# Kernel optimization log

Measured on AMD Instinct MI355X. Metric: run time of the kernel, lower is better.

Reference implementation:

```python
import jax, jax.numpy as jnp
import numpy as np

N, C, H, O, NUM_CLASSES = 4096, 768, 512, 50, 1


def setup_inputs() -> dict:
    key = jax.random.key(0)
    ks = jax.random.split(key, 8)
    x = jax.random.normal(ks[0], (N, C), dtype=jnp.float32)
    labels = jax.random.randint(ks[1], (N,), 0, 2, dtype=jnp.int64)
    W1 = jax.random.normal(ks[2], (C, H), dtype=jnp.float32) / np.sqrt(C)
    b1 = jnp.zeros((H,), dtype=jnp.float32)
    W2 = jax.random.normal(ks[3], (H, O), dtype=jnp.float32) / np.sqrt(H)
    b2 = jnp.zeros((O,), dtype=jnp.float32)
    fcW = jax.random.normal(ks[4], (C + O, NUM_CLASSES), dtype=jnp.float32) / np.sqrt(C + O)
    fcb = jnp.zeros((NUM_CLASSES,), dtype=jnp.float32)
    return {"x": x, "labels": labels, "W1": W1, "b1": b1, "W2": W2, "b2": b2, "fcW": fcW, "fcb": fcb}


def _build_graph(x, labels):
    # similarity-threshold edge construction (dense masked form of the python double loop)
    sim = x @ x.T                                   # [N, N]
    n = x.shape[0]
    diff = labels[:, None] != labels[None, :]       # cross-label pairs
    cnt = jnp.sum(diff)
    s = jnp.sum(jnp.where(diff, sim, 0.0))
    threshold = jnp.where(cnt > 0, s / cnt.astype(sim.dtype), jnp.asarray(0.0, sim.dtype))
    eye = jnp.eye(n, dtype=bool)
    same = (labels[:, None] == labels[None, :]) & ~eye
    edge_mask = same & (sim <= threshold)           # symmetric (sim symmetric)
    loss_mask = edge_mask & (jnp.arange(n)[:, None] < jnp.arange(n)[None, :])  # i<j pairs
    adj = jax.lax.stop_gradient(edge_mask.astype(x.dtype))
    # GCN normalization with self-loops
    a = adj + jnp.eye(n, dtype=x.dtype)
    dinv = jax.lax.rsqrt(jnp.sum(a, axis=1))        # deg >= 1
    norm_adj = dinv[:, None] * a * dinv[None, :]
    return norm_adj, loss_mask


def reference(x, labels, W1, b1, W2, b2, fcW, fcb):
    norm_adj, loss_mask = _build_graph(x, labels)
    h = jax.nn.relu(norm_adj @ (x @ W1) + b1)       # conv1 + relu
    g = norm_adj @ (h @ W2) + b2                    # conv2
    f_g = jnp.concatenate([x, g], axis=-1)          # [N, C+O]
    out = f_g @ fcW + fcb                           # [N, 1]
    return out, f_g, loss_mask, x
```

## Files before the change

### kernel.cpp

```cpp
#include <hip/hip_runtime.h>
#include <hip/hip_bf16.h>
#include <math.h>

#define NN 4096
#define CD 768
#define HD 512
#define OD 50
#define FGD 818

typedef short short8 __attribute__((ext_vector_type(8)));
typedef float f32x4 __attribute__((ext_vector_type(4)));
typedef unsigned short us4 __attribute__((ext_vector_type(4)));
typedef unsigned short ushortT;
typedef unsigned char uchar;

__device__ inline ushortT f2bf(float v) {
    __hip_bfloat16 b = __float2bfloat16(v);
    return *(ushortT*)&b;
}
__device__ inline float bf2f(ushortT u) {
    __hip_bfloat16 b = *(__hip_bfloat16*)&u;
    return __bfloat162float(b);
}
__device__ inline float dinv_of(int d) {
    return (float)(1.0 / sqrt((double)(1 + d)));
}

__global__ __launch_bounds__(256) void gsum_kernel(const float* __restrict__ x,
                                                   const int* __restrict__ labels,
                                                   double* __restrict__ gsum) {
    int b = blockIdx.x;
    int t = threadIdx.x;
    double a0[3] = {0, 0, 0}, a1[3] = {0, 0, 0};
    for (int rr = 0; rr < 16; ++rr) {
        int row = b * 16 + rr;
        int lab = labels[row];
#pragma unroll
        for (int s = 0; s < 3; ++s) {
            double v = (double)x[(size_t)row * CD + t + s * 256];
            if (lab == 0) a0[s] += v; else a1[s] += v;
        }
    }
#pragma unroll
    for (int s = 0; s < 3; ++s) {
        atomicAdd(&gsum[t + s * 256], a0[s]);
        atomicAdd(&gsum[768 + t + s * 256], a1[s]);
    }
}

__global__ __launch_bounds__(256) void gdot_kernel(const double* __restrict__ gsum,
                                                   const int* __restrict__ labels,
                                                   double* __restrict__ scal) {
    int t = threadIdx.x;
    double d = 0.0;
    for (int c = t; c < CD; c += 256) d += gsum[c] * gsum[768 + c];
    int n0 = 0;
    for (int i = t; i < NN; i += 256) n0 += (labels[i] == 0) ? 1 : 0;
    for (int off = 32; off; off >>= 1) {
        d += __shfl_down(d, off);
        n0 += __shfl_down(n0, off);
    }
    __shared__ double sd[4];
    __shared__ int sn[4];
    int wid = t >> 6, lane = t & 63;
    if (lane == 0) { sd[wid] = d; sn[wid] = n0; }
    __syncthreads();
    if (t == 0) {
        double D = sd[0] + sd[1] + sd[2] + sd[3];
        double N0 = (double)(sn[0] + sn[1] + sn[2] + sn[3]);
        scal[0] = 2.0 * D;
        scal[1] = 2.0 * N0 * ((double)NN - N0);
    }
}

#define BAND 4e-3
#define RC_CAP (1 << 18)

__global__ __launch_bounds__(256) void sim_fused(
    const ushortT* __restrict__ xh, const ushortT* __restrict__ xl,
    const int* __restrict__ labels, const double* __restrict__ scal,
    ushortT* __restrict__ ab, float* __restrict__ lm, int* __restrict__ deg,
    int* __restrict__ rc_cnt, int* __restrict__ rc_list) {
    int t = blockIdx.x;
    int by = (int)((129.0 - sqrt(16641.0 - 8.0 * (double)t)) * 0.5);
    while (by * (129 - by) / 2 > t) --by;
    while ((by + 1) * (129 - (by + 1)) / 2 <= t) ++by;
    int bx = by + (t - by * (129 - by) / 2);
    bool diag = (bx == by);

    __shared__ ushortT lds[4 * 64 * 72];
    __shared__ int larr[128];
    int tid = threadIdx.x;
    int lane = tid & 63;
    int w = tid >> 6;
    int wr = w >> 1, wc = w & 1;
    int m = lane & 15, quad = lane >> 4;
    int row0 = by * 64, col0 = bx * 64;

    if (tid < 64) larr[tid] = labels[row0 + tid];
    else if (tid < 128) larr[tid] = labels[col0 + tid - 64];

    f32x4 acc[2][2] = {{{0.f, 0.f, 0.f, 0.f}, {0.f, 0.f, 0.f, 0.f}},
                       {{0.f, 0.f, 0.f, 0.f}, {0.f, 0.f, 0.f, 0.f}}};

    for (int k0 = 0; k0 < CD; k0 += 64) {
#pragma unroll
        for (int tt = 0; tt < 2; ++tt) {
            int id2 = tid + tt * 256;
            int row = id2 >> 3, c8 = (id2 & 7) * 8;
            *(short8*)&lds[0 * 4608 + row * 72 + c8] =
                *(const short8*)&xh[(size_t)(row0 + row) * CD + k0 + c8];
            *(short8*)&lds[1 * 4608 + row * 72 + c8] =
                *(const short8*)&xl[(size_t)(row0 + row) * CD + k0 + c8];
            *(short8*)&lds[2 * 4608 + row * 72 + c8] =
                *(const short8*)&xh[(size_t)(col0 + row) * CD + k0 + c8];
            *(short8*)&lds[3 * 4608 + row * 72 + c8] =
                *(const short8*)&xl[(size_t)(col0 + row) * CD + k0 + c8];
        }
        __syncthreads();
#pragma unroll
        for (int ks = 0; ks < 2; ++ks) {
            short8 ah[2], al[2], bh[2], bl[2];
#pragma unroll
            for (int i = 0; i < 2; ++i) {
                int ro = (wr * 32 + i * 16 + m) * 72 + ks * 32 + quad * 8;
                ah[i] = *(const short8*)&lds[0 * 4608 + ro];
                al[i] = *(const short8*)&lds[1 * 4608 + ro];
            }
#pragma unroll
            for (int j = 0; j < 2; ++j) {
                int co = (wc * 32 + j * 16 + m) * 72 + ks * 32 + quad * 8;
                bh[j] = *(const short8*)&lds[2 * 4608 + co];
                bl[j] = *(const short8*)&lds[3 * 4608 + co];
            }
#pragma unroll
            for (int i = 0; i < 2; ++i)
#pragma unroll
                for (int j = 0; j < 2; ++j) {
                    acc[i][j] = __builtin_amdgcn_mfma_f32_16x16x32_bf16(
                        ah[i], bh[j], acc[i][j], 0, 0, 0);
                    acc[i][j] = __builtin_amdgcn_mfma_f32_16x16x32_bf16(
                        ah[i], bl[j], acc[i][j], 0, 0, 0);
                    acc[i][j] = __builtin_amdgcn_mfma_f32_16x16x32_bf16(
                        al[i], bh[j], acc[i][j], 0, 0, 0);
                }
        }
        __syncthreads();
    }

    double thrd;
    {
        double cnt = scal[1];
        thrd = (cnt > 0.0) ? (scal[0] / cnt) : 0.0;
    }
    uchar* flags = (uchar*)lds;
#pragma unroll
    for (int i = 0; i < 2; ++i)
#pragma unroll
        for (int j = 0; j < 2; ++j) {
#pragma unroll
            for (int r = 0; r < 4; ++r) {
                int row = wr * 32 + i * 16 + quad * 4 + r;
                int col = wc * 32 + j * 16 + m;
                bool same = (larr[row] == larr[64 + col]);
                bool selfp = ((row0 + row) == (col0 + col));
                bool edge = false;
                if (same && !selfp) {
                    double s = (double)acc[i][j][r];
                    if (s <= thrd - BAND) {
                        edge = true;
                    } else if (s <= thrd + BAND) {
                        edge = (s <= thrd);
                        int enc = ((row0 + row) << 12) | (col0 + col) |
                                  (diag ? 0 : (1 << 24)) |
                                  (edge ? (1 << 25) : 0);
                        int idx = atomicAdd(rc_cnt, 1);
                        if (idx < RC_CAP) rc_list[idx] = enc;
                    }
                }
                flags[row * 68 + col] = edge ? 1 : 0;
            }
        }
    __syncthreads();

    {
        int r = tid >> 2, q = tid & 3;
        int cnti = 0;
#pragma unroll
        for (int s = 0; s < 4; ++s) {
            int cb = q * 16 + s * 4;
            float4 f;
            us4 a4;
#pragma unroll
            for (int k2 = 0; k2 < 4; ++k2) {
                int c = cb + k2;
                bool fl = flags[r * 68 + c] != 0;
                cnti += fl ? 1 : 0;
                ((ushortT*)&a4)[k2] =
                    (fl || (diag && r == c)) ? (ushortT)0x3F80 : (ushortT)0;
                ((float*)&f)[k2] = (fl && (row0 + r < col0 + c)) ? 1.0f : 0.0f;
            }
            *(us4*)&ab[(size_t)(row0 + r) * NN + col0 + cb] = a4;
            *(float4*)&lm[(size_t)(row0 + r) * NN + col0 + cb] = f;
        }
        cnti += __shfl_down(cnti, 1);
        cnti += __shfl_down(cnti, 2);
        if (q == 0 && cnti) atomicAdd(&deg[row0 + r], cnti);
    }

    if (!diag) {
        int c = tid >> 2, q = tid & 3;
        int cnti = 0;
        float4 fz = {0.0f, 0.0f, 0.0f, 0.0f};
#pragma unroll
        for (int s = 0; s < 4; ++s) {
            int rb = q * 16 + s * 4;
            us4 a4;
#pragma unroll
            for (int k2 = 0; k2 < 4; ++k2) {
                bool fl = flags[(rb + k2) * 68 + c] != 0;
                cnti += fl ? 1 : 0;
                ((ushortT*)&a4)[k2] = fl ? (ushortT)0x3F80 : (ushortT)0;
            }
            *(us4*)&ab[(size_t)(col0 + c) * NN + row0 + rb] = a4;
            *(float4*)&lm[(size_t)(col0 + c) * NN + row0 + rb] = fz;
        }
        cnti += __shfl_down(cnti, 1);
        cnti += __shfl_down(cnti, 2);
        if (q == 0 && cnti) atomicAdd(&deg[col0 + c], cnti);
    }
}

__global__ __launch_bounds__(256) void rc_fix(
    const float* __restrict__ x, const double* __restrict__ scal,
    const int* __restrict__ rc_cnt, const int* __restrict__ rc_list,
    ushortT* __restrict__ ab, float* __restrict__ lm, int* __restrict__ deg) {
    int cnt = *rc_cnt;
    if (cnt > RC_CAP) cnt = RC_CAP;
    double thrd;
    {
        double c = scal[1];
        thrd = (c > 0.0) ? (scal[0] / c) : 0.0;
    }
    int lane = threadIdx.x & 63;
    int wid = (blockIdx.x * 256 + threadIdx.x) >> 6;
    int nw = (gridDim.x * 256) >> 6;
    for (int e = wid; e < cnt; e += nw) {
        int enc = rc_list[e];
        int c = enc & 0xFFF;
        int r = (enc >> 12) & 0xFFF;
        bool mirror = (enc >> 24) & 1;
        bool prov = (enc >> 25) & 1;
        const float* xi = x + (size_t)r * CD;
        const float* xj = x + (size_t)c * CD;
        double d = 0.0;
#pragma unroll
        for (int s = 0; s < 12; ++s)
            d += (double)xi[lane + s * 64] * (double)xj[lane + s * 64];
        for (int off = 32; off; off >>= 1) d += __shfl_down(d, off);
        if (lane == 0) {
            bool exact = (d <= thrd);
            if (exact != prov) {
                ushortT av = exact ? (ushortT)0x3F80 : (ushortT)0;
                ab[(size_t)r * NN + c] = av;
                lm[(size_t)r * NN + c] = (exact && r < c) ? 1.0f : 0.0f;
                int dlt = exact ? 1 : -1;
                atomicAdd(&deg[r], dlt);
                if (mirror) {
                    ab[(size_t)c * NN + r] = av;
                    atomicAdd(&deg[c], dlt);
                }
            }
        }
    }
}

__global__ __launch_bounds__(256) void prep_kernel(
    const float* __restrict__ x, const float* __restrict__ W1,
    const float* __restrict__ W2, float* __restrict__ fg, float* __restrict__ xo,
    ushortT* __restrict__ xh, ushortT* __restrict__ xl, ushortT* __restrict__ w1t,
    ushortT* __restrict__ w2t) {
    int b = blockIdx.x;
    if (b < 4096) {
        int t = threadIdx.x;
        if (t < 192) {
            float4 v = *(const float4*)&x[(size_t)b * CD + t * 4];
            *(float4*)&xo[(size_t)b * CD + t * 4] = v;
            fg[(size_t)b * FGD + t * 4 + 0] = v.x;
            fg[(size_t)b * FGD + t * 4 + 1] = v.y;
            fg[(size_t)b * FGD + t * 4 + 2] = v.z;
            fg[(size_t)b * FGD + t * 4 + 3] = v.w;
            us4 hh, ll;
            float* vp = (float*)&v;
#pragma unroll
            for (int k = 0; k < 4; ++k) {
                ushortT h = f2bf(vp[k]);
                ((ushortT*)&hh)[k] = h;
                ((ushortT*)&ll)[k] = f2bf(vp[k] - bf2f(h));
            }
            *(us4*)&xh[(size_t)b * CD + t * 4] = hh;
            *(us4*)&xl[(size_t)b * CD + t * 4] = ll;
        }
        return;
    }
    __shared__ float tT[32][33];
    const float* P;
    ushortT* T;
    int K, N, Npad, k0, n0;
    if (b < 4480) {
        int bb = b - 4096;
        P = W1; T = w1t; K = CD; N = HD; Npad = HD;
        k0 = (bb % 24) * 32; n0 = (bb / 24) * 32;
    } else {
        int bb = b - 4480;
        P = W2; T = w2t; K = HD; N = OD; Npad = 64;
        k0 = (bb % 16) * 32; n0 = (bb / 16) * 32;
    }
    int tx = threadIdx.x & 31, ty = threadIdx.x >> 5;
#pragma unroll
    for (int s = 0; s < 4; ++s) {
        int k = k0 + ty + s * 8, n = n0 + tx;
        tT[ty + s * 8][tx] = (k < K && n < N) ? P[(size_t)k * N + n] : 0.0f;
    }
    __syncthreads();
#pragma unroll
    for (int s = 0; s < 4; ++s) {
        int n = n0 + ty + s * 8, k = k0 + tx;
        if (n < Npad && k < K) T[(size_t)n * K + k] = f2bf(tT[tx][ty + s * 8]);
    }
}

template <bool RELU, bool HASBIAS, int EPI>
__global__ __launch_bounds__(256) void gemm_bf16(
    const ushortT* __restrict__ A, const ushortT* __restrict__ B,
    ushortT* __restrict__ Cb, int M, int Nn, int K, int ldc,
    const int* __restrict__ deg, const float* __restrict__ bias) {
    __shared__ ushortT lds[2 * 64 * 72];
    int tid = threadIdx.x;
    int lane = tid & 63;
    int w = tid >> 6;
    int wr = w >> 1, wc = w & 1;
    int m = lane & 15, quad = lane >> 4;
    int row0 = blockIdx.y * 64, col0 = blockIdx.x * 64;

    f32x4 acc[2][2] = {{{0.f, 0.f, 0.f, 0.f}, {0.f, 0.f, 0.f, 0.f}},
                       {{0.f, 0.f, 0.f, 0.f}, {0.f, 0.f, 0.f, 0.f}}};

    for (int k0 = 0; k0 < K; k0 += 64) {
#pragma unroll
        for (int t = 0; t < 2; ++t) {
            int id2 = tid + t * 256;
            int row = id2 >> 3, c8 = (id2 & 7) * 8;
            *(short8*)&lds[row * 72 + c8] =
                *(const short8*)&A[(size_t)(row0 + row) * K + k0 + c8];
            *(short8*)&lds[4608 + row * 72 + c8] =
                *(const short8*)&B[(size_t)(col0 + row) * K + k0 + c8];
        }
        __syncthreads();
#pragma unroll
        for (int ks = 0; ks < 2; ++ks) {
            short8 af[2], bf[2];
#pragma unroll
            for (int i = 0; i < 2; ++i)
                af[i] = *(const short8*)&lds[(wr * 32 + i * 16 + m) * 72 +
                                             ks * 32 + quad * 8];
#pragma unroll
            for (int j = 0; j < 2; ++j)
                bf[j] = *(const short8*)&lds[4608 + (wc * 32 + j * 16 + m) * 72 +
                                             ks * 32 + quad * 8];
#pragma unroll
            for (int i = 0; i < 2; ++i)
#pragma unroll
                for (int j = 0; j < 2; ++j)
                    acc[i][j] = __builtin_amdgcn_mfma_f32_16x16x32_bf16(
                        af[i], bf[j], acc[i][j], 0, 0, 0);
        }
        __syncthreads();
    }

    if (EPI == 2) {
        ushortT* Th = lds;
#pragma unroll
        for (int i = 0; i < 2; ++i)
#pragma unroll
            for (int j = 0; j < 2; ++j)
#pragma unroll
                for (int r = 0; r < 4; ++r) {
                    int row = wr * 32 + i * 16 + quad * 4 + r;
                    int col = wc * 32 + j * 16 + m;
                    float dv = dinv_of(deg[row0 + row]);
                    Th[col * 72 + row] = f2bf(acc[i][j][r] * dv);
                }
        __syncthreads();
#pragma unroll
        for (int t = 0; t < 2; ++t) {
            int id2 = tid + t * 256;
            int cc = id2 >> 3, chunk = id2 & 7;
            *(short8*)&Cb[(size_t)(col0 + cc) * M + row0 + chunk * 8] =
                *(const short8*)&Th[cc * 72 + chunk * 8];
        }
    } else {
#pragma unroll
        for (int i = 0; i < 2; ++i)
#pragma unroll
            for (int j = 0; j < 2; ++j)
#pragma unroll
                for (int r = 0; r < 4; ++r) {
                    int row = wr * 32 + i * 16 + quad * 4 + r;
                    int col = wc * 32 + j * 16 + m;
                    int gr = row0 + row, gc = col0 + col;
                    if (gc < Nn) {
                        float v = acc[i][j][r] * dinv_of(deg[gr]);
                        if (HASBIAS) v += bias[gc];
                        if (RELU) v = fmaxf(v, 0.0f);
                        Cb[(size_t)gr * ldc + gc] = f2bf(v);
                    }
                }
    }
}

__global__ __launch_bounds__(256) void gemm_part(
    const ushortT* __restrict__ A, const ushortT* __restrict__ B,
    float* __restrict__ P, int M, int K, int KC) {
    __shared__ ushortT lds[2 * 64 * 72];
    int tid = threadIdx.x;
    int lane = tid & 63;
    int w = tid >> 6;
    int wr = w >> 1, wc = w & 1;
    int m = lane & 15, quad = lane >> 4;
    int kb = blockIdx.x;
    int row0 = blockIdx.y * 64;
    int kbase = kb * KC;

    f32x4 acc[2][2] = {{{0.f, 0.f, 0.f, 0.f}, {0.f, 0.f, 0.f, 0.f}},
                       {{0.f, 0.f, 0.f, 0.f}, {0.f, 0.f, 0.f, 0.f}}};

    for (int k0 = 0; k0 < KC; k0 += 64) {
#pragma unroll
        for (int t = 0; t < 2; ++t) {
            int id2 = tid + t * 256;
            int row = id2 >> 3, c8 = (id2 & 7) * 8;
            *(short8*)&lds[row * 72 + c8] =
                *(const short8*)&A[(size_t)(row0 + row) * K + kbase + k0 + c8];
            *(short8*)&lds[4608 + row * 72 + c8] =
                *(const short8*)&B[(size_t)row * K + kbase + k0 + c8];
        }
        __syncthreads();
#pragma unroll
        for (int ks = 0; ks < 2; ++ks) {
            short8 af[2], bf[2];
#pragma unroll
            for (int i = 0; i < 2; ++i)
                af[i] = *(const short8*)&lds[(wr * 32 + i * 16 + m) * 72 +
                                             ks * 32 + quad * 8];
#pragma unroll
            for (int j = 0; j < 2; ++j)
                bf[j] = *(const short8*)&lds[4608 + (wc * 32 + j * 16 + m) * 72 +
                                             ks * 32 + quad * 8];
#pragma unroll
            for (int i = 0; i < 2; ++i)
#pragma unroll
                for (int j = 0; j < 2; ++j)
                    acc[i][j] = __builtin_amdgcn_mfma_f32_16x16x32_bf16(
                        af[i], bf[j], acc[i][j], 0, 0, 0);
        }
        __syncthreads();
    }
#pragma unroll
    for (int i = 0; i < 2; ++i)
#pragma unroll
        for (int j = 0; j < 2; ++j)
#pragma unroll
            for (int r = 0; r < 4; ++r) {
                int row = wr * 32 + i * 16 + quad * 4 + r;
                int col = wc * 32 + j * 16 + m;
                P[((size_t)kb * M + row0 + row) * 64 + col] = acc[i][j][r];
            }
}

__global__ __launch_bounds__(256) void gemm_partW(
    const ushortT* __restrict__ A, const ushortT* __restrict__ B,
    float* __restrict__ P, int M, int K, int KC, int ldP) {
    __shared__ ushortT lds[2 * 64 * 72];
    int tid = threadIdx.x;
    int lane = tid & 63;
    int w = tid >> 6;
    int wr = w >> 1, wc = w & 1;
    int m = lane & 15, quad = lane >> 4;
    int col0 = blockIdx.x * 64;
    int row0 = blockIdx.y * 64;
    int kb = blockIdx.z;
    int kbase = kb * KC;

    f32x4 acc[2][2] = {{{0.f, 0.f, 0.f, 0.f}, {0.f, 0.f, 0.f, 0.f}},
                       {{0.f, 0.f, 0.f, 0.f}, {0.f, 0.f, 0.f, 0.f}}};

    for (int k0 = 0; k0 < KC; k0 += 64) {
#pragma unroll
        for (int t = 0; t < 2; ++t) {
            int id2 = tid + t * 256;
            int row = id2 >> 3, c8 = (id2 & 7) * 8;
            *(short8*)&lds[row * 72 + c8] =
                *(const short8*)&A[(size_t)(row0 + row) * K + kbase + k0 + c8];
            *(short8*)&lds[4608 + row * 72 + c8] =
                *(const short8*)&B[(size_t)(col0 + row) * K + kbase + k0 + c8];
        }
        __syncthreads();
#pragma unroll
        for (int ks = 0; ks < 2; ++ks) {
            short8 af[2], bf[2];
#pragma unroll
            for (int i = 0; i < 2; ++i)
                af[i] = *(const short8*)&lds[(wr * 32 + i * 16 + m) * 72 +
                                             ks * 32 + quad * 8];
#pragma unroll
            for (int j = 0; j < 2; ++j)
                bf[j] = *(const short8*)&lds[4608 + (wc * 32 + j * 16 + m) * 72 +
                                             ks * 32 + quad * 8];
#pragma unroll
            for (int i = 0; i < 2; ++i)
#pragma unroll
                for (int j = 0; j < 2; ++j)
                    acc[i][j] = __builtin_amdgcn_mfma_f32_16x16x32_bf16(
                        af[i], bf[j], acc[i][j], 0, 0, 0);
        }
        __syncthreads();
    }
#pragma unroll
    for (int i = 0; i < 2; ++i)
#pragma unroll
        for (int j = 0; j < 2; ++j)
#pragma unroll
            for (int r = 0; r < 4; ++r) {
                int row = wr * 32 + i * 16 + quad * 4 + r;
                int col = wc * 32 + j * 16 + m;
                P[((size_t)kb * M + row0 + row) * ldP + col0 + col] =
                    acc[i][j][r];
            }
}

__global__ __launch_bounds__(256) void k5_epi(const float* __restrict__ P5,
                                              const int* __restrict__ deg,
                                              const float* __restrict__ b1,
                                              ushortT* __restrict__ hb) {
    int tid = threadIdx.x;
    int cg = tid & 127;
    int rr = tid >> 7;
#pragma unroll
    for (int p = 0; p < 2; ++p) {
        int r = blockIdx.x * 4 + p * 2 + rr;
        float dv = dinv_of(deg[r]);
        float4 s = {0.f, 0.f, 0.f, 0.f};
#pragma unroll
        for (int kb = 0; kb < 4; ++kb) {
            float4 v = *(const float4*)&P5[((size_t)kb * NN + r) * HD + cg * 4];
            s.x += v.x; s.y += v.y; s.z += v.z; s.w += v.w;
        }
        float4 bv = *(const float4*)&b1[cg * 4];
        us4 o;
        o[0] = f2bf(fmaxf(s.x * dv + bv.x, 0.f));
        o[1] = f2bf(fmaxf(s.y * dv + bv.y, 0.f));
        o[2] = f2bf(fmaxf(s.z * dv + bv.z, 0.f));
        o[3] = f2bf(fmaxf(s.w * dv + bv.w, 0.f));
        *(us4*)&hb[(size_t)r * HD + cg * 4] = o;
    }
}

__global__ __launch_bounds__(256) void k6_epi(const float* __restrict__ P6,
                                              const int* __restrict__ deg,
                                              ushortT* __restrict__ hw2sT) {
    __shared__ ushortT Th[64 * 72];
    int row0 = blockIdx.x * 64;
    int tid = threadIdx.x;
    int rl = tid >> 2, q = tid & 3;
    float dv = dinv_of(deg[row0 + rl]);
#pragma unroll
    for (int s = 0; s < 16; ++s) {
        int c = q * 16 + s;
        float v = 0.f;
#pragma unroll
        for (int kb = 0; kb < 4; ++kb)
            v += P6[((size_t)kb * NN + row0 + rl) * 64 + c];
        Th[c * 72 + rl] = f2bf(v * dv);
    }
    __syncthreads();
#pragma unroll
    for (int t = 0; t < 2; ++t) {
        int id2 = tid + t * 256;
        int cc = id2 >> 3, chunk = id2 & 7;
        *(short8*)&hw2sT[(size_t)cc * NN + row0 + chunk * 8] =
            *(const short8*)&Th[cc * 72 + chunk * 8];
    }
}

__global__ __launch_bounds__(256) void k7_epi_out(
    const float* __restrict__ P7, const int* __restrict__ deg,
    const float* __restrict__ b2, const float* __restrict__ fcW,
    const float* __restrict__ fcb, float* __restrict__ fg,
    float* __restrict__ out) {
    int row0 = blockIdx.x * 64;
    int tid = threadIdx.x;
    int rl = tid >> 2, q = tid & 3;
    int r = row0 + rl;
    float dv = dinv_of(deg[r]);
    float sg = 0.f;
#pragma unroll
    for (int s = 0; s < 16; ++s) {
        int c = q * 16 + s;
        if (c < OD) {
            float v = 0.f;
#pragma unroll
            for (int kb = 0; kb < 8; ++kb)
                v += P7[((size_t)kb * NN + r) * 64 + c];
            v = v * dv + b2[c];
            fg[(size_t)r * FGD + CD + c] = v;
            sg += v * fcW[CD + c];
        }
    }
    const float* fr = fg + (size_t)r * FGD;
    float sx = 0.f;
    for (int k = q * 192; k < (q + 1) * 192; k += 2) {
        float2 vv = *(const float2*)&fr[k];
        float2 ww = *(const float2*)&fcW[k];
        sx += vv.x * ww.x + vv.y * ww.y;
    }
    float s = sx + sg;
    s += __shfl_down(s, 1);
    s += __shfl_down(s, 2);
    if (q == 0) out[r] = s + fcb[0];
}

extern "C" void kernel_launch(void* const* d_in, const int* in_sizes, int n_in,
                              void* d_out, int out_size, void* d_ws, size_t ws_size,
                              hipStream_t stream) {
    const float* x = (const float*)d_in[0];
    const int* labels = (const int*)d_in[1];
    const float* W1 = (const float*)d_in[2];
    const float* b1 = (const float*)d_in[3];
    const float* W2 = (const float*)d_in[4];
    const float* b2 = (const float*)d_in[5];
    const float* fcW = (const float*)d_in[6];
    const float* fcb = (const float*)d_in[7];
    float* outp = (float*)d_out;

    const size_t o_out = 0;
    const size_t o_fg = 4096;
    const size_t o_lm = o_fg + (size_t)NN * FGD;
    const size_t o_x = o_lm + (size_t)NN * NN;

    char* ws = (char*)d_ws;
    size_t off = 0;
    ushortT* ab = (ushortT*)(ws + off); off += (size_t)NN * NN * 2;
    ushortT* xh = (ushortT*)(ws + off); off += (size_t)NN * CD * 2;
    ushortT* xl = (ushortT*)(ws + off); off += (size_t)NN * CD * 2;
    ushortT* w1t = (ushortT*)(ws + off); off += (size_t)HD * CD * 2;
    ushortT* xw1sT = (ushortT*)(ws + off); off += (size_t)HD * NN * 2;
    ushortT* hb = (ushortT*)(ws + off); off += (size_t)NN * HD * 2;
    ushortT* w2t = (ushortT*)(ws + off); off += (size_t)64 * HD * 2;
    ushortT* hw2sT = (ushortT*)(ws + off); off += (size_t)64 * NN * 2;
    char* zbase = ws + off;
    int* deg = (int*)(ws + off); off += (size_t)NN * 4;
    double* gsum = (double*)(ws + off); off += 1536 * 8;
    double* scal = (double*)(ws + off); off += 16;
    int* rc_cnt = (int*)(ws + off); off += 16;
    size_t zbytes = (size_t)NN * 4 + 1536 * 8 + 16 + 16;
    char* uni = ws + off;
    int* rc_list = (int*)uni;
    float* P5 = (float*)uni;
    float* P6 = (float*)uni;
    float* P7 = (float*)uni;
    off += (size_t)4 * NN * HD * 4;

    hipMemsetAsync(zbase, 0, zbytes, stream);

    prep_kernel<<<4512, 256, 0, stream>>>(x, W1, W2, outp + o_fg, outp + o_x, xh, xl,
                                          w1t, w2t);

    gsum_kernel<<<256, 256, 0, stream>>>(x, labels, gsum);
    gdot_kernel<<<1, 256, 0, stream>>>(gsum, labels, scal);

    sim_fused<<<2080, 256, 0, stream>>>(xh, xl, labels, scal, ab, outp + o_lm, deg,
                                        rc_cnt, rc_list);

    rc_fix<<<512, 256, 0, stream>>>(x, scal, rc_cnt, rc_list, ab, outp + o_lm, deg);

    gemm_bf16<false, false, 2><<<dim3(HD / 64, NN / 64), 256, 0, stream>>>(
        xh, w1t, xw1sT, NN, HD, CD, 0, deg, nullptr);

    gemm_partW<<<dim3(HD / 64, NN / 64, 4), 256, 0, stream>>>(
        ab, xw1sT, P5, NN, NN, NN / 4, HD);
    k5_epi<<<NN / 4, 256, 0, stream>>>(P5, deg, b1, hb);

    gemm_part<<<dim3(4, NN / 64), 256, 0, stream>>>(hb, w2t, P6, NN, HD, HD / 4);
    k6_epi<<<NN / 64, 256, 0, stream>>>(P6, deg, hw2sT);

    gemm_part<<<dim3(8, NN / 64), 256, 0, stream>>>(ab, hw2sT, P7, NN, NN, NN / 8);
    k7_epi_out<<<NN / 64, 256, 0, stream>>>(P7, deg, b2, fcW, fcb, outp + o_fg,
                                            outp + o_out);
}
```

Measured before the change: 354.8 us.

## Store adjacency as packed bitmask and expand to bf16 inside GEMM loaders

The dense bf16 adjacency matrix (32 MB) is replaced by a 1-bit-per-entry packed u64 bitmask (2 MB). The similarity kernel now writes these bits, and the fixup kernel updates them with atomicOr and atomicAnd. Both adjacency GEMMs expand the bits to bf16 1.0/0.0 in LDS while staging tiles. This cuts the traffic of writing the adjacency once and reading it twice, at the cost of extra ALU work for unpacking and 64-bit atomics in the fixup path.

```diff
diff --git a/kernel.cpp b/kernel.cpp
--- a/kernel.cpp
+++ b/kernel.cpp
@@ -13,6 +13,7 @@
 typedef unsigned short us4 __attribute__((ext_vector_type(4)));
 typedef unsigned short ushortT;
 typedef unsigned char uchar;
+typedef unsigned long long u64;
 
 __device__ inline ushortT f2bf(float v) {
     __hip_bfloat16 b = __float2bfloat16(v);
@@ -79,7 +80,7 @@
 __global__ __launch_bounds__(256) void sim_fused(
     const ushortT* __restrict__ xh, const ushortT* __restrict__ xl,
     const int* __restrict__ labels, const double* __restrict__ scal,
-    ushortT* __restrict__ ab, float* __restrict__ lm, int* __restrict__ deg,
+    u64* __restrict__ abbits, float* __restrict__ lm, int* __restrict__ deg,
     int* __restrict__ rc_cnt, int* __restrict__ rc_list) {
     int t = blockIdx.x;
     int by = (int)((129.0 - sqrt(16641.0 - 8.0 * (double)t)) * 0.5);
@@ -186,55 +187,68 @@
     {
         int r = tid >> 2, q = tid & 3;
         int cnti = 0;
+        unsigned int bits16 = 0;
 #pragma unroll
         for (int s = 0; s < 4; ++s) {
             int cb = q * 16 + s * 4;
             float4 f;
-            us4 a4;
 #pragma unroll
             for (int k2 = 0; k2 < 4; ++k2) {
                 int c = cb + k2;
                 bool fl = flags[r * 68 + c] != 0;
                 cnti += fl ? 1 : 0;
-                ((ushortT*)&a4)[k2] =
-                    (fl || (diag && r == c)) ? (ushortT)0x3F80 : (ushortT)0;
+                if (fl || (diag && r == c)) bits16 |= 1u << (s * 4 + k2);
                 ((float*)&f)[k2] = (fl && (row0 + r < col0 + c)) ? 1.0f : 0.0f;
             }
-            *(us4*)&ab[(size_t)(row0 + r) * NN + col0 + cb] = a4;
             *(float4*)&lm[(size_t)(row0 + r) * NN + col0 + cb] = f;
         }
+        unsigned int s1 = __shfl_down(bits16, 1);
+        unsigned int s2 = __shfl_down(bits16, 2);
+        unsigned int s3 = __shfl_down(bits16, 3);
         cnti += __shfl_down(cnti, 1);
         cnti += __shfl_down(cnti, 2);
-        if (q == 0 && cnti) atomicAdd(&deg[row0 + r], cnti);
+        if (q == 0) {
+            u64 u = (u64)bits16 | ((u64)s1 << 16) | ((u64)s2 << 32) |
+                    ((u64)s3 << 48);
+            abbits[(size_t)(row0 + r) * 64 + bx] = u;
+            if (cnti) atomicAdd(&deg[row0 + r], cnti);
+        }
     }
 
     if (!diag) {
         int c = tid >> 2, q = tid & 3;
         int cnti = 0;
+        unsigned int bits16 = 0;
         float4 fz = {0.0f, 0.0f, 0.0f, 0.0f};
 #pragma unroll
         for (int s = 0; s < 4; ++s) {
             int rb = q * 16 + s * 4;
-            us4 a4;
 #pragma unroll
             for (int k2 = 0; k2 < 4; ++k2) {
                 bool fl = flags[(rb + k2) * 68 + c] != 0;
                 cnti += fl ? 1 : 0;
-                ((ushortT*)&a4)[k2] = fl ? (ushortT)0x3F80 : (ushortT)0;
-            }
-            *(us4*)&ab[(size_t)(col0 + c) * NN + row0 + rb] = a4;
+                if (fl) bits16 |= 1u << (s * 4 + k2);
+            }
             *(float4*)&lm[(size_t)(col0 + c) * NN + row0 + rb] = fz;
         }
+        unsigned int s1 = __shfl_down(bits16, 1);
+        unsigned int s2 = __shfl_down(bits16, 2);
+        unsigned int s3 = __shfl_down(bits16, 3);
         cnti += __shfl_down(cnti, 1);
         cnti += __shfl_down(cnti, 2);
-        if (q == 0 && cnti) atomicAdd(&deg[col0 + c], cnti);
+        if (q == 0) {
+            u64 u = (u64)bits16 | ((u64)s1 << 16) | ((u64)s2 << 32) |
+                    ((u64)s3 << 48);
+            abbits[(size_t)(col0 + c) * 64 + by] = u;
+            if (cnti) atomicAdd(&deg[col0 + c], cnti);
+        }
     }
 }
 
 __global__ __launch_bounds__(256) void rc_fix(
     const float* __restrict__ x, const double* __restrict__ scal,
     const int* __restrict__ rc_cnt, const int* __restrict__ rc_list,
-    ushortT* __restrict__ ab, float* __restrict__ lm, int* __restrict__ deg) {
+    u64* __restrict__ abbits, float* __restrict__ lm, int* __restrict__ deg) {
     int cnt = *rc_cnt;
     if (cnt > RC_CAP) cnt = RC_CAP;
     double thrd;
@@ -261,13 +275,16 @@
         if (lane == 0) {
             bool exact = (d <= thrd);
             if (exact != prov) {
-                ushortT av = exact ? (ushortT)0x3F80 : (ushortT)0;
-                ab[(size_t)r * NN + c] = av;
+                u64 mk = 1ull << (c & 63);
+                if (exact) atomicOr(&abbits[(size_t)r * 64 + (c >> 6)], mk);
+                else       atomicAnd(&abbits[(size_t)r * 64 + (c >> 6)], ~mk);
                 lm[(size_t)r * NN + c] = (exact && r < c) ? 1.0f : 0.0f;
                 int dlt = exact ? 1 : -1;
                 atomicAdd(&deg[r], dlt);
                 if (mirror) {
-                    ab[(size_t)c * NN + r] = av;
+                    u64 mk2 = 1ull << (r & 63);
+                    if (exact) atomicOr(&abbits[(size_t)c * 64 + (r >> 6)], mk2);
+                    else       atomicAnd(&abbits[(size_t)c * 64 + (r >> 6)], ~mk2);
                     atomicAdd(&deg[c], dlt);
                 }
             }
@@ -478,8 +495,80 @@
             }
 }
 
-__global__ __launch_bounds__(256) void gemm_partW(
-    const ushortT* __restrict__ A, const ushortT* __restrict__ B,
+__global__ __launch_bounds__(256) void gemm_partB(
+    const u64* __restrict__ Abits, const ushortT* __restrict__ B,
+    float* __restrict__ P, int M, int K, int KC) {
+    __shared__ ushortT lds[2 * 64 * 72];
+    int tid = threadIdx.x;
+    int lane = tid & 63;
+    int w = tid >> 6;
+    int wr = w >> 1, wc = w & 1;
+    int m = lane & 15, quad = lane >> 4;
+    int kb = blockIdx.x;
+    int row0 = blockIdx.y * 64;
+    int kbase = kb * KC;
+    int er = tid >> 2, eq = tid & 3;
+
+    f32x4 acc[2][2] = {{{0.f, 0.f, 0.f, 0.f}, {0.f, 0.f, 0.f, 0.f}},
+                       {{0.f, 0.f, 0.f, 0.f}, {0.f, 0.f, 0.f, 0.f}}};
+
+    for (int k0 = 0; k0 < KC; k0 += 64) {
+#pragma unroll
+        for (int t = 0; t < 2; ++t) {
+            int id2 = tid + t * 256;
+            int row = id2 >> 3, c8 = (id2 & 7) * 8;
+            *(short8*)&lds[4608 + row * 72 + c8] =
+                *(const short8*)&B[(size_t)row * K + kbase + k0 + c8];
+        }
+        {
+            u64 bits = Abits[(size_t)(row0 + er) * 64 + ((kbase + k0) >> 6)];
+            unsigned int half = (unsigned int)(bits >> (eq * 16)) & 0xFFFFu;
+            short8 v0, v1;
+#pragma unroll
+            for (int k = 0; k < 8; ++k) {
+                ((ushortT*)&v0)[k] =
+                    ((half >> k) & 1) ? (ushortT)0x3F80 : (ushortT)0;
+                ((ushortT*)&v1)[k] =
+                    ((half >> (k + 8)) & 1) ? (ushortT)0x3F80 : (ushortT)0;
+            }
+            *(short8*)&lds[er * 72 + eq * 16] = v0;
+            *(short8*)&lds[er * 72 + eq * 16 + 8] = v1;
+        }
+        __syncthreads();
+#pragma unroll
+        for (int ks = 0; ks < 2; ++ks) {
+            short8 af[2], bf[2];
+#pragma unroll
+            for (int i = 0; i < 2; ++i)
+                af[i] = *(const short8*)&lds[(wr * 32 + i * 16 + m) * 72 +
+                                             ks * 32 + quad * 8];
+#pragma unroll
+            for (int j = 0; j < 2; ++j)
+                bf[j] = *(const short8*)&lds[4608 + (wc * 32 + j * 16 + m) * 72 +
+                                             ks * 32 + quad * 8];
+#pragma unroll
+            for (int i = 0; i < 2; ++i)
+#pragma unroll
+                for (int j = 0; j < 2; ++j)
+                    acc[i][j] = __builtin_amdgcn_mfma_f32_16x16x32_bf16(
+                        af[i], bf[j], acc[i][j], 0, 0, 0);
+        }
+        __syncthreads();
+    }
+#pragma unroll
+    for (int i = 0; i < 2; ++i)
+#pragma unroll
+        for (int j = 0; j < 2; ++j)
+#pragma unroll
+            for (int r = 0; r < 4; ++r) {
+                int row = wr * 32 + i * 16 + quad * 4 + r;
+                int col = wc * 32 + j * 16 + m;
+                P[((size_t)kb * M + row0 + row) * 64 + col] = acc[i][j][r];
+            }
+}
+
+__global__ __launch_bounds__(256) void gemm_partWB(
+    const u64* __restrict__ Abits, const ushortT* __restrict__ B,
     float* __restrict__ P, int M, int K, int KC, int ldP) {
     __shared__ ushortT lds[2 * 64 * 72];
     int tid = threadIdx.x;
@@ -491,6 +580,7 @@
     int row0 = blockIdx.y * 64;
     int kb = blockIdx.z;
     int kbase = kb * KC;
+    int er = tid >> 2, eq = tid & 3;
 
     f32x4 acc[2][2] = {{{0.f, 0.f, 0.f, 0.f}, {0.f, 0.f, 0.f, 0.f}},
                        {{0.f, 0.f, 0.f, 0.f}, {0.f, 0.f, 0.f, 0.f}}};
@@ -500,10 +590,22 @@
         for (int t = 0; t < 2; ++t) {
             int id2 = tid + t * 256;
             int row = id2 >> 3, c8 = (id2 & 7) * 8;
-            *(short8*)&lds[row * 72 + c8] =
-                *(const short8*)&A[(size_t)(row0 + row) * K + kbase + k0 + c8];
             *(short8*)&lds[4608 + row * 72 + c8] =
                 *(const short8*)&B[(size_t)(col0 + row) * K + kbase + k0 + c8];
+        }
+        {
+            u64 bits = Abits[(size_t)(row0 + er) * 64 + ((kbase + k0) >> 6)];
+            unsigned int half = (unsigned int)(bits >> (eq * 16)) & 0xFFFFu;
+            short8 v0, v1;
+#pragma unroll
+            for (int k = 0; k < 8; ++k) {
+                ((ushortT*)&v0)[k] =
+                    ((half >> k) & 1) ? (ushortT)0x3F80 : (ushortT)0;
+                ((ushortT*)&v1)[k] =
+                    ((half >> (k + 8)) & 1) ? (ushortT)0x3F80 : (ushortT)0;
+            }
+            *(short8*)&lds[er * 72 + eq * 16] = v0;
+            *(short8*)&lds[er * 72 + eq * 16 + 8] = v1;
         }
         __syncthreads();
 #pragma unroll
@@ -650,7 +752,7 @@
 
     char* ws = (char*)d_ws;
     size_t off = 0;
-    ushortT* ab = (ushortT*)(ws + off); off += (size_t)NN * NN * 2;
+    u64* abbits = (u64*)(ws + off); off += (size_t)NN * 64 * 8;
     ushortT* xh = (ushortT*)(ws + off); off += (size_t)NN * CD * 2;
     ushortT* xl = (ushortT*)(ws + off); off += (size_t)NN * CD * 2;
     ushortT* w1t = (ushortT*)(ws + off); off += (size_t)HD * CD * 2;
@@ -679,22 +781,24 @@
     gsum_kernel<<<256, 256, 0, stream>>>(x, labels, gsum);
     gdot_kernel<<<1, 256, 0, stream>>>(gsum, labels, scal);
 
-    sim_fused<<<2080, 256, 0, stream>>>(xh, xl, labels, scal, ab, outp + o_lm, deg,
-                                        rc_cnt, rc_list);
-
-    rc_fix<<<512, 256, 0, stream>>>(x, scal, rc_cnt, rc_list, ab, outp + o_lm, deg);
+    sim_fused<<<2080, 256, 0, stream>>>(xh, xl, labels, scal, abbits, outp + o_lm,
+                                        deg, rc_cnt, rc_list);
+
+    rc_fix<<<512, 256, 0, stream>>>(x, scal, rc_cnt, rc_list, abbits, outp + o_lm,
+                                    deg);
 
     gemm_bf16<false, false, 2><<<dim3(HD / 64, NN / 64), 256, 0, stream>>>(
         xh, w1t, xw1sT, NN, HD, CD, 0, deg, nullptr);
 
-    gemm_partW<<<dim3(HD / 64, NN / 64, 4), 256, 0, stream>>>(
-        ab, xw1sT, P5, NN, NN, NN / 4, HD);
+    gemm_partWB<<<dim3(HD / 64, NN / 64, 4), 256, 0, stream>>>(
+        abbits, xw1sT, P5, NN, NN, NN / 4, HD);
     k5_epi<<<NN / 4, 256, 0, stream>>>(P5, deg, b1, hb);
 
     gemm_part<<<dim3(4, NN / 64), 256, 0, stream>>>(hb, w2t, P6, NN, HD, HD / 4);
     k6_epi<<<NN / 64, 256, 0, stream>>>(P6, deg, hw2sT);
 
-    gemm_part<<<dim3(8, NN / 64), 256, 0, stream>>>(ab, hw2sT, P7, NN, NN, NN / 8);
+    gemm_partB<<<dim3(8, NN / 64), 256, 0, stream>>>(abbits, hw2sT, P7, NN, NN,
+                                                     NN / 8);
     k7_epi_out<<<NN / 64, 256, 0, stream>>>(P7, deg, b2, fcW, fcb, outp + o_fg,
                                             outp + o_out);
 }
```

Measured after the change: 332.9 us. 1.07x faster.
